# Kernel optimization log

Measured on AMD Instinct MI355X. Metric: run time of the kernel, lower is better.

Reference implementation:

```python
import jax, jax.numpy as jnp
import numpy as np

EMB_DIM = 1024
N_HEADS = 16
HEAD_DIM = EMB_DIM // N_HEADS


def setup_inputs() -> dict:
    key = jax.random.key(0)
    ks = jax.random.split(key, 6)
    B, T, C = 2, 2048, EMB_DIM
    s = 1.0 / np.sqrt(C)
    return {
        "x": jax.random.normal(ks[0], (B, T, C), dtype=jnp.float32),
        "W_query": jax.random.normal(ks[1], (C, C), dtype=jnp.float32) * s,
        "W_key": jax.random.normal(ks[2], (C, C), dtype=jnp.float32) * s,
        "W_value": jax.random.normal(ks[3], (C, C), dtype=jnp.float32) * s,
        "W_out": jax.random.normal(ks[4], (C, C), dtype=jnp.float32) * s,
        "b_out": jax.random.normal(ks[5], (C,), dtype=jnp.float32) * 0.01,
    }


def reference(x, W_query, W_key, W_value, W_out, b_out):
    # x: [B, T, C]. Linear weights stored as [in, out] (transposed torch layout).
    B, T, C = x.shape
    H, D = N_HEADS, HEAD_DIM

    def split_heads(t):  # [B,T,C] -> [B,H,T,D]
        return t.reshape(B, T, H, D).transpose(0, 2, 1, 3)

    q = split_heads(x @ W_query)
    k = split_heads(x @ W_key)
    v = split_heads(x @ W_value)

    scale = 1.0 / jnp.sqrt(jnp.asarray(D, dtype=x.dtype))
    att = jnp.einsum("bhqd,bhkd->bhqk", q, k) * scale  # [B,H,T,T]
    causal = jnp.tril(jnp.ones((T, T), dtype=bool))
    att = jnp.where(causal[None, None], att, jnp.asarray(-jnp.inf, dtype=att.dtype))
    att = jax.nn.softmax(att, axis=-1)
    # dropout is identity in eval / drop_rate=0
    y = jnp.einsum("bhqk,bhkd->bhqd", att, v)  # [B,H,T,D]
    y = y.transpose(0, 2, 1, 3).reshape(B, T, C)
    return y @ W_out + b_out
```

## Files before the change

kernel.cpp:

```cpp
#include <hip/hip_runtime.h>
#include <hip/hip_bf16.h>
#include <math.h>

#define Bsz 2
#define Tsz 2048
#define Csz 1024
#define Hsz 16
#define Dsz 64

typedef __attribute__((ext_vector_type(8))) short frag8;
typedef __attribute__((ext_vector_type(4))) float f4;
typedef __attribute__((ext_vector_type(8))) unsigned short us8;
typedef __attribute__((ext_vector_type(4))) _Float16 frag4h;
typedef __attribute__((ext_vector_type(8))) _Float16 frag8h;

static __device__ __forceinline__ unsigned short f2bf(float f) {
  union { __hip_bfloat16 h; unsigned short u; } c;
  c.h = __float2bfloat16(f);
  return c.u;
}
static __device__ __forceinline__ unsigned short f2h(float f) {
  union { _Float16 h; unsigned short u; } c;
  c.h = (_Float16)f;
  return c.u;
}

#define GLDS16(g, l)                                                        \
  __builtin_amdgcn_global_load_lds(                                         \
      (const __attribute__((address_space(1))) void*)(g),                   \
      (__attribute__((address_space(3))) void*)(l), 16, 0, 0)

#define QSCALE 0.18033688f

__global__ __launch_bounds__(256) void cast_x(const float* __restrict__ x,
                                              unsigned short* __restrict__ xb) {
  const int i = (blockIdx.x * 256 + threadIdx.x) * 8;
  const float4 a = *(const float4*)(x + i);
  const float4 b = *(const float4*)(x + i + 4);
  us8 v;
  v[0] = f2bf(a.x); v[1] = f2bf(a.y); v[2] = f2bf(a.z); v[3] = f2bf(a.w);
  v[4] = f2bf(b.x); v[5] = f2bf(b.y); v[6] = f2bf(b.z); v[7] = f2bf(b.w);
  *(us8*)(xb + i) = v;
}

__global__ __launch_bounds__(256) void transpose_cast(
    const float* __restrict__ s0, const float* __restrict__ s1,
    const float* __restrict__ s2, const float* __restrict__ s3,
    unsigned short* __restrict__ d0, unsigned short* __restrict__ d1,
    unsigned short* __restrict__ d2, unsigned short* __restrict__ d3) {
  __shared__ float Ls[64][65];
  const int mat = blockIdx.x >> 8;
  const int tile = blockIdx.x & 255;
  const float* src = mat == 0 ? s0 : mat == 1 ? s1 : mat == 2 ? s2 : s3;
  unsigned short* dst = mat == 0 ? d0 : mat == 1 ? d1 : mat == 2 ? d2 : d3;
  const int tr0 = (tile >> 4) << 6, tc0 = (tile & 15) << 6;
  const int t = threadIdx.x;
  const int lr = t >> 4, lc = (t & 15) << 2;
#pragma unroll
  for (int j = 0; j < 4; ++j) {
    const float4 v = *(const float4*)(src + (size_t)(tr0 + lr + j * 16) * 1024 + tc0 + lc);
    Ls[lr + j * 16][lc + 0] = v.x;
    Ls[lr + j * 16][lc + 1] = v.y;
    Ls[lr + j * 16][lc + 2] = v.z;
    Ls[lr + j * 16][lc + 3] = v.w;
  }
  __syncthreads();
#pragma unroll
  for (int j = 0; j < 4; ++j) {
    ushort4 v;
    v.x = f2bf(Ls[lc + 0][lr + j * 16]);
    v.y = f2bf(Ls[lc + 1][lr + j * 16]);
    v.z = f2bf(Ls[lc + 2][lr + j * 16]);
    v.w = f2bf(Ls[lc + 3][lr + j * 16]);
    *(ushort4*)(dst + (size_t)(tc0 + lr + j * 16) * 1024 + tr0 + lc) = v;
  }
}

template <int MODE, int MT>
__global__ __launch_bounds__(256) void mm_bt(
    const unsigned short* __restrict__ A, const unsigned short* __restrict__ Bt,
    const float* __restrict__ bias, unsigned short* __restrict__ O0,
    unsigned short* __restrict__ O1, unsigned short* __restrict__ O2,
    float* __restrict__ Of) {
  __shared__ __align__(16) unsigned short As[MT * 32 * 64];
  __shared__ __align__(16) unsigned short Bs[128 * 64];
  const int K = 1024;
  const int tid = threadIdx.x;
  const int wave = tid >> 6, lane = tid & 63;
  const int quad = lane >> 4, l16 = lane & 15;
  const int wrow = (wave >> 1) * (MT * 16), wn = wave & 1;
  const int row0 = blockIdx.y * (MT * 32), col0 = blockIdx.x << 7;

  const int sr = lane >> 3, sg = lane & 7;
  const int g0 = sg ^ sr;
  const unsigned short* gA = A + (size_t)(row0 + wave * (MT * 8) + sr) * K + (g0 << 3);
  const unsigned short* gB = Bt + (size_t)(col0 + wave * 32 + sr) * K + (g0 << 3);

  f4 acc[MT][4];
#pragma unroll
  for (int i = 0; i < MT; ++i)
#pragma unroll
    for (int j = 0; j < 4; ++j) acc[i][j] = (f4){0.f, 0.f, 0.f, 0.f};

  for (int kk = 0; kk < K; kk += 64) {
    __syncthreads();
#pragma unroll
    for (int s = 0; s < MT; ++s)
      GLDS16(gA + kk + (size_t)(s * 8) * K, &As[(wave * (MT * 8) + s * 8) * 64]);
#pragma unroll
    for (int s = 0; s < 4; ++s)
      GLDS16(gB + kk + (size_t)(s * 8) * K, &Bs[(wave * 32 + s * 8) * 64]);
    __syncthreads();

#pragma unroll
    for (int ks = 0; ks < 2; ++ks) {
      frag8 af[MT], bf[4];
#pragma unroll
      for (int mt = 0; mt < MT; ++mt) {
        const int r = wrow + mt * 16 + l16;
        af[mt] = *(const frag8*)&As[r * 64 + (((ks * 4 + quad) ^ (l16 & 7)) << 3)];
      }
#pragma unroll
      for (int nt = 0; nt < 4; ++nt) {
        const int n = wn * 64 + nt * 16 + l16;
        bf[nt] = *(const frag8*)&Bs[n * 64 + (((ks * 4 + quad) ^ (l16 & 7)) << 3)];
      }
#pragma unroll
      for (int mt = 0; mt < MT; ++mt)
#pragma unroll
        for (int nt = 0; nt < 4; ++nt)
          acc[mt][nt] = __builtin_amdgcn_mfma_f32_16x16x32_bf16(af[mt], bf[nt], acc[mt][nt], 0, 0, 0);
    }
  }

  if (MODE == 0) {
    if (col0 < 2048) {
      const bool isK = (col0 >= 1024);
      unsigned short* dst = isK ? O1 : O0;
      const float sc = isK ? 1.0f : QSCALE;
#pragma unroll
      for (int mt = 0; mt < MT; ++mt)
#pragma unroll
        for (int nt = 0; nt < 4; ++nt) {
          const int m = row0 + wrow + mt * 16 + quad * 4;
          const int n = (col0 & 1023) + wn * 64 + nt * 16 + l16;
          const int b = m >> 11, h = n >> 6, d = n & 63;
#pragma unroll
          for (int r = 0; r < 4; ++r) {
            const int tk = (m + r) & (Tsz - 1);
            dst[(((size_t)b * Hsz + h) * Tsz + tk) * Dsz + d] = f2bf(acc[mt][nt][r] * sc);
          }
        }
    } else {
#pragma unroll
      for (int mt = 0; mt < MT; ++mt)
#pragma unroll
        for (int nt = 0; nt < 4; ++nt) {
          const int tok = row0 + wrow + mt * 16 + quad * 4;
          const int ch = (col0 - 2048) + wn * 64 + nt * 16 + l16;
          const int b = tok >> 11, tk = tok & (Tsz - 1);
          const int h = ch >> 6, d = ch & 63;
          const int t5 = tk & 31;
          const int pos = (tk & ~31) + ((t5 >> 4) << 2) + (((t5 >> 2) & 3) << 3) + (t5 & 3);
          ushort4 v;
          v.x = f2h(acc[mt][nt][0]); v.y = f2h(acc[mt][nt][1]);
          v.z = f2h(acc[mt][nt][2]); v.w = f2h(acc[mt][nt][3]);
          *(ushort4*)&O2[(((size_t)b * Hsz + h) * Dsz + d) * Tsz + pos] = v;
        }
    }
  } else {
#pragma unroll
    for (int mt = 0; mt < MT; ++mt)
#pragma unroll
      for (int nt = 0; nt < 4; ++nt) {
        const int m = row0 + wrow + mt * 16 + quad * 4;
        const int n = col0 + wn * 64 + nt * 16 + l16;
        const float bv = bias[n];
#pragma unroll
        for (int r = 0; r < 4; ++r)
          Of[(size_t)(m + r) * Csz + n] = acc[mt][nt][r] + bv;
      }
  }
}

__global__ __launch_bounds__(256, 2) void attn_mfma(
    const unsigned short* __restrict__ Qb,
    const unsigned short* __restrict__ Kb,
    const unsigned short* __restrict__ VTb,
    unsigned short* __restrict__ Y) {
  __shared__ __align__(16) unsigned short SM[4][2][4096];

  const int tid = threadIdx.x;
  const int sp = tid >> 6, lane = tid & 63;
  const int quad = lane >> 4, l16 = lane & 15;

  const int bh = blockIdx.x & 31;
  const int j = 63 - (blockIdx.x >> 5);
  const int qb0 = j << 5;

  const unsigned short* Qh = Qb + (size_t)bh * Tsz * Dsz;
  const unsigned short* Kh = Kb + (size_t)bh * Tsz * Dsz;
  const unsigned short* Vh = VTb + (size_t)bh * Dsz * Tsz;

  const int sr = lane >> 3, sg = lane & 7;
  const unsigned short* gK = Kh + (size_t)sr * Dsz + ((sg ^ sr) << 3);
  const int vr = lane >> 2, vc = lane & 3;
  const unsigned short* gV = Vh + (size_t)vr * Tsz + ((vc ^ ((vr + (vr >> 2)) & 3)) << 3);

  frag8 qf[2][2];
#pragma unroll
  for (int m = 0; m < 2; ++m)
#pragma unroll
    for (int ks = 0; ks < 2; ++ks)
      qf[m][ks] = *(const frag8*)(Qh + (size_t)(qb0 + m * 16 + l16) * Dsz + ks * 32 + quad * 8);
  asm volatile("s_waitcnt vmcnt(0)" ::: "memory");

  f4 o[2][4];
  float lsum[2] = {0.f, 0.f};
#pragma unroll
  for (int m = 0; m < 2; ++m)
#pragma unroll
    for (int nt = 0; nt < 4; ++nt) o[m][nt] = (f4){0.f, 0.f, 0.f, 0.f};
  const f4 zf = (f4){0.f, 0.f, 0.f, 0.f};
  const int fl = (l16 + (l16 >> 2)) & 3;

  const int nc = (j >= sp) ? ((j - sp) >> 2) + 1 : 0;

  auto STAGE = [&](int bb, int cc) {
#pragma unroll
    for (int g = 0; g < 4; ++g)
      GLDS16(gK + (size_t)cc * 2048 + g * 512, &SM[sp][bb][g * 512]);
#pragma unroll
    for (int g = 0; g < 4; ++g)
      GLDS16(gV + (size_t)g * 16 * Tsz + cc * 32, &SM[sp][bb][2048 + g * 512]);
  };

  if (nc > 0) STAGE(0, sp);
  if (nc > 1) STAGE(1, sp + 4);

  for (int i = 0; i < nc; ++i) {
    const int c = sp + 4 * i;
    const int bsel = i & 1;
    if (i + 1 < nc) asm volatile("s_waitcnt vmcnt(8)" ::: "memory");
    else            asm volatile("s_waitcnt vmcnt(0)" ::: "memory");

    const unsigned short* Kl = &SM[sp][bsel][0];
    const unsigned short* Vl = &SM[sp][bsel][2048];
    frag8 kf[2][2];
#pragma unroll
    for (int n = 0; n < 2; ++n)
#pragma unroll
      for (int ks = 0; ks < 2; ++ks)
        kf[n][ks] = *(const frag8*)&Kl[(n * 16 + l16) * 64 + (((ks * 4 + quad) ^ (l16 & 7)) << 3)];
    frag8h vf[4];
#pragma unroll
    for (int nt = 0; nt < 4; ++nt)
      vf[nt] = *(const frag8h*)&Vl[(nt * 16 + l16) * 32 + ((quad ^ fl) << 3)];

    f4 st[2][2];
#pragma unroll
    for (int n = 0; n < 2; ++n)
#pragma unroll
      for (int m = 0; m < 2; ++m) {
        f4 a = __builtin_amdgcn_mfma_f32_16x16x32_bf16(kf[n][0], qf[m][0], zf, 0, 0, 0);
        st[n][m] = __builtin_amdgcn_mfma_f32_16x16x32_bf16(kf[n][1], qf[m][1], a, 0, 0, 0);
      }

    if (i + 2 < nc) {
      asm volatile("s_waitcnt lgkmcnt(0)" ::: "memory");
      STAGE(bsel, c + 8);
    }

    const bool dm = (c == j);
    frag4h paf[2][2];
#pragma unroll
    for (int m = 0; m < 2; ++m) {
      const int qq = m * 16 + l16;
#pragma unroll
      for (int n = 0; n < 2; ++n) {
        const int key0 = n * 16 + quad * 4;
        float p[4];
#pragma unroll
        for (int r = 0; r < 4; ++r) {
          float sv = st[n][m][r];
          if (dm && (key0 + r > qq)) sv = -INFINITY;
          p[r] = __builtin_amdgcn_exp2f(sv);
        }
        lsum[m] += (p[0] + p[1]) + (p[2] + p[3]);
        frag4h ph;
        ph[0] = (_Float16)p[0]; ph[1] = (_Float16)p[1];
        ph[2] = (_Float16)p[2]; ph[3] = (_Float16)p[3];
        paf[m][n] = ph;
      }
    }
#pragma unroll
    for (int m = 0; m < 2; ++m)
#pragma unroll
      for (int nt = 0; nt < 4; ++nt) {
        const frag4h vlo = __builtin_shufflevector(vf[nt], vf[nt], 0, 1, 2, 3);
        const frag4h vhi = __builtin_shufflevector(vf[nt], vf[nt], 4, 5, 6, 7);
        f4 a = __builtin_amdgcn_mfma_f32_16x16x16f16(paf[m][0], vlo, o[m][nt], 0, 0, 0);
        o[m][nt] = __builtin_amdgcn_mfma_f32_16x16x16f16(paf[m][1], vhi, a, 0, 0, 0);
      }
  }

  __syncthreads();
  float* comb = (float*)SM;
  float* cp = comb + (size_t)((sp - 1) * 64 + lane) * 37;
  if (sp != 0) {
#pragma unroll
    for (int m = 0; m < 2; ++m)
#pragma unroll
      for (int nt = 0; nt < 4; ++nt)
        *(f4*)(cp + m * 16 + nt * 4) = o[m][nt];
    cp[32] = lsum[0]; cp[33] = lsum[1];
  }
  __syncthreads();
  if (sp == 0) {
#pragma unroll
    for (int s = 0; s < 3; ++s) {
      const float* rp = comb + (size_t)(s * 64 + lane) * 37;
#pragma unroll
      for (int m = 0; m < 2; ++m)
#pragma unroll
        for (int nt = 0; nt < 4; ++nt)
          o[m][nt] += *(const f4*)(rp + m * 16 + nt * 4);
      lsum[0] += rp[32]; lsum[1] += rp[33];
    }

#pragma unroll
    for (int m = 0; m < 2; ++m) {
      lsum[m] += __shfl_xor(lsum[m], 16);
      lsum[m] += __shfl_xor(lsum[m], 32);
    }
    const int b = bh >> 4, h = bh & 15;
#pragma unroll
    for (int m = 0; m < 2; ++m)
#pragma unroll
      for (int r = 0; r < 4; ++r) {
        const float inv = 1.f / __shfl(lsum[m], quad * 4 + r);
        const int tk = qb0 + m * 16 + quad * 4 + r;
        unsigned short* yp = Y + ((size_t)b * Tsz + tk) * Csz + h * 64 + l16;
#pragma unroll
        for (int nt = 0; nt < 4; ++nt)
          yp[nt * 16] = f2bf(o[m][nt][r] * inv);
      }
  }
}

extern "C" void kernel_launch(void* const* d_in, const int* in_sizes, int n_in,
                              void* d_out, int out_size, void* d_ws, size_t ws_size,
                              hipStream_t stream) {
  const float* x  = (const float*)d_in[0];
  const float* Wq = (const float*)d_in[1];
  const float* Wk = (const float*)d_in[2];
  const float* Wv = (const float*)d_in[3];
  const float* Wo = (const float*)d_in[4];
  const float* bo = (const float*)d_in[5];

  const size_t NEL = (size_t)Bsz * Tsz * Csz;
  const size_t WSZ = (size_t)Csz * Csz;
  unsigned short* xb  = (unsigned short*)d_ws;
  unsigned short* WT  = xb + NEL;
  unsigned short* WoT = WT + 3 * WSZ;
  unsigned short* Qb  = WoT + WSZ;
  unsigned short* Kb  = Qb + NEL;
  unsigned short* VTb = Kb + NEL;
  unsigned short* Yb  = VTb + NEL;

  cast_x<<<NEL / 2048, 256, 0, stream>>>(x, xb);
  transpose_cast<<<1024, 256, 0, stream>>>(Wq, Wk, Wv, Wo,
                                           WT, WT + WSZ, WT + 2 * WSZ, WoT);

  mm_bt<0, 4><<<dim3(24, 32), 256, 0, stream>>>(xb, WT, nullptr, Qb, Kb, VTb, nullptr);

  attn_mfma<<<2048, 256, 0, stream>>>(Qb, Kb, VTb, Yb);

  mm_bt<2, 2><<<dim3(8, 64), 256, 0, stream>>>(Yb, WoT, bo, nullptr, nullptr, nullptr,
                                               (float*)d_out);
}
```

Baseline: 186.9 us.

## Load V fragments directly from global and raise attention occupancy

The attention kernel stops staging V tiles through LDS and instead loads each lane's V fragment straight from global memory into registers. Only K stays double-buffered in shared memory, which halves the LDS footprint and lets launch bounds rise from 2 to 4 blocks per CU. The causal mask is also split into a separate diagonal-block path, so off-diagonal blocks skip the per-element compare. The risks are that the direct V loads are less coalesced, and that the vmcnt-based wait now depends on compiler-inserted waits when only one K stage is outstanding.

```diff
diff --git a/kernel.cpp b/kernel.cpp
--- a/kernel.cpp
+++ b/kernel.cpp
@@ -183,12 +183,12 @@
   }
 }
 
-__global__ __launch_bounds__(256, 2) void attn_mfma(
+__global__ __launch_bounds__(256, 4) void attn_mfma(
     const unsigned short* __restrict__ Qb,
     const unsigned short* __restrict__ Kb,
     const unsigned short* __restrict__ VTb,
     unsigned short* __restrict__ Y) {
-  __shared__ __align__(16) unsigned short SM[4][2][4096];
+  __shared__ __align__(16) unsigned short SMK[4][2][2048];
 
   const int tid = threadIdx.x;
   const int sp = tid >> 6, lane = tid & 63;
@@ -204,8 +204,7 @@
 
   const int sr = lane >> 3, sg = lane & 7;
   const unsigned short* gK = Kh + (size_t)sr * Dsz + ((sg ^ sr) << 3);
-  const int vr = lane >> 2, vc = lane & 3;
-  const unsigned short* gV = Vh + (size_t)vr * Tsz + ((vc ^ ((vr + (vr >> 2)) & 3)) << 3);
+  const unsigned short* vl = Vh + (size_t)l16 * Tsz + quad * 8;
 
   frag8 qf[2][2];
 #pragma unroll
@@ -222,40 +221,42 @@
 #pragma unroll
     for (int nt = 0; nt < 4; ++nt) o[m][nt] = (f4){0.f, 0.f, 0.f, 0.f};
   const f4 zf = (f4){0.f, 0.f, 0.f, 0.f};
-  const int fl = (l16 + (l16 >> 2)) & 3;
 
   const int nc = (j >= sp) ? ((j - sp) >> 2) + 1 : 0;
 
-  auto STAGE = [&](int bb, int cc) {
+  auto STAGEK = [&](int bb, int cc) {
 #pragma unroll
     for (int g = 0; g < 4; ++g)
-      GLDS16(gK + (size_t)cc * 2048 + g * 512, &SM[sp][bb][g * 512]);
-#pragma unroll
-    for (int g = 0; g < 4; ++g)
-      GLDS16(gV + (size_t)g * 16 * Tsz + cc * 32, &SM[sp][bb][2048 + g * 512]);
+      GLDS16(gK + (size_t)cc * 2048 + g * 512, &SMK[sp][bb][g * 512]);
   };
 
-  if (nc > 0) STAGE(0, sp);
-  if (nc > 1) STAGE(1, sp + 4);
+  if (nc > 0) {
+    STAGEK(0, sp);
+    STAGEK(1, nc > 1 ? sp + 4 : sp);
+  }
 
   for (int i = 0; i < nc; ++i) {
     const int c = sp + 4 * i;
     const int bsel = i & 1;
-    if (i + 1 < nc) asm volatile("s_waitcnt vmcnt(8)" ::: "memory");
-    else            asm volatile("s_waitcnt vmcnt(0)" ::: "memory");
-
-    const unsigned short* Kl = &SM[sp][bsel][0];
-    const unsigned short* Vl = &SM[sp][bsel][2048];
+    asm volatile("s_waitcnt vmcnt(4)" ::: "memory");
+
+    const unsigned short* Kl = &SMK[sp][bsel][0];
     frag8 kf[2][2];
 #pragma unroll
     for (int n = 0; n < 2; ++n)
 #pragma unroll
       for (int ks = 0; ks < 2; ++ks)
         kf[n][ks] = *(const frag8*)&Kl[(n * 16 + l16) * 64 + (((ks * 4 + quad) ^ (l16 & 7)) << 3)];
+
     frag8h vf[4];
 #pragma unroll
     for (int nt = 0; nt < 4; ++nt)
-      vf[nt] = *(const frag8h*)&Vl[(nt * 16 + l16) * 32 + ((quad ^ fl) << 3)];
+      vf[nt] = *(const frag8h*)(vl + (size_t)(nt * 16) * Tsz + (c << 5));
+
+    if (i + 2 < nc) {
+      asm volatile("s_waitcnt lgkmcnt(0)" ::: "memory");
+      STAGEK(bsel, c + 8);
+    }
 
     f4 st[2][2];
 #pragma unroll
@@ -266,33 +267,44 @@
         st[n][m] = __builtin_amdgcn_mfma_f32_16x16x32_bf16(kf[n][1], qf[m][1], a, 0, 0, 0);
       }
 
-    if (i + 2 < nc) {
-      asm volatile("s_waitcnt lgkmcnt(0)" ::: "memory");
-      STAGE(bsel, c + 8);
-    }
-
-    const bool dm = (c == j);
     frag4h paf[2][2];
-#pragma unroll
-    for (int m = 0; m < 2; ++m) {
-      const int qq = m * 16 + l16;
-#pragma unroll
-      for (int n = 0; n < 2; ++n) {
-        const int key0 = n * 16 + quad * 4;
-        float p[4];
-#pragma unroll
-        for (int r = 0; r < 4; ++r) {
-          float sv = st[n][m][r];
-          if (dm && (key0 + r > qq)) sv = -INFINITY;
-          p[r] = __builtin_amdgcn_exp2f(sv);
+    if (c == j) {
+#pragma unroll
+      for (int m = 0; m < 2; ++m) {
+        const int qq = m * 16 + l16;
+#pragma unroll
+        for (int n = 0; n < 2; ++n) {
+          const int key0 = n * 16 + quad * 4;
+          float p[4];
+#pragma unroll
+          for (int r = 0; r < 4; ++r) {
+            float sv = st[n][m][r];
+            if (key0 + r > qq) sv = -INFINITY;
+            p[r] = __builtin_amdgcn_exp2f(sv);
+          }
+          lsum[m] += (p[0] + p[1]) + (p[2] + p[3]);
+          frag4h ph;
+          ph[0] = (_Float16)p[0]; ph[1] = (_Float16)p[1];
+          ph[2] = (_Float16)p[2]; ph[3] = (_Float16)p[3];
+          paf[m][n] = ph;
         }
-        lsum[m] += (p[0] + p[1]) + (p[2] + p[3]);
-        frag4h ph;
-        ph[0] = (_Float16)p[0]; ph[1] = (_Float16)p[1];
-        ph[2] = (_Float16)p[2]; ph[3] = (_Float16)p[3];
-        paf[m][n] = ph;
-      }
-    }
+      }
+    } else {
+#pragma unroll
+      for (int m = 0; m < 2; ++m)
+#pragma unroll
+        for (int n = 0; n < 2; ++n) {
+          float p[4];
+#pragma unroll
+          for (int r = 0; r < 4; ++r) p[r] = __builtin_amdgcn_exp2f(st[n][m][r]);
+          lsum[m] += (p[0] + p[1]) + (p[2] + p[3]);
+          frag4h ph;
+          ph[0] = (_Float16)p[0]; ph[1] = (_Float16)p[1];
+          ph[2] = (_Float16)p[2]; ph[3] = (_Float16)p[3];
+          paf[m][n] = ph;
+        }
+    }
+
 #pragma unroll
     for (int m = 0; m < 2; ++m)
 #pragma unroll
@@ -305,7 +317,7 @@
   }
 
   __syncthreads();
-  float* comb = (float*)SM;
+  float* comb = (float*)SMK;
   float* cp = comb + (size_t)((sp - 1) * 64 + lane) * 37;
   if (sp != 0) {
 #pragma unroll
```

New measurement: 190.5 us. About the same (+1.9%).
